# Kernel tuning notes

Hardware: AMD Instinct MI355X
Metric: run time of the kernel (lower is better)

The kernel has to match this reference:

```python
import jax, jax.numpy as jnp
import numpy as np


def setup_inputs() -> dict:
    key = jax.random.key(0)
    k1, k2 = jax.random.split(key)
    sites = jax.random.normal(k1, (4096, 128), dtype=jnp.float32)
    consensus = jax.random.normal(k2, (512, 128), dtype=jnp.float32)
    return {"sites": sites, "consensus": consensus}


def reference(sites, consensus):
    # Broadcast L1 distance: [N, 1, d] - [1, M, d] -> reduce |.| over d -> [N, M]
    dist = jnp.sum(jnp.abs(sites[:, None, :] - consensus[None, :, :]), axis=-1)
    # softmax over consensus axis of negated distances
    return jax.nn.softmax(-dist, axis=-1)
```

## Files before the change

kernel.cpp:

```cpp
#include <hip/hip_runtime.h>

#define N_SITES 4096
#define M_CONS  512
#define DIM     128
#define RPB     8
#define CH      16
#define NCH     8
#define QPC     4

__global__ __launch_bounds__(512, 1) void fused_kernel(const float* __restrict__ sites,
                                                       const float* __restrict__ cons,
                                                       float* __restrict__ out) {
    __shared__ __align__(16) float lds[16384];

    const int tid = threadIdx.x;
    const int bid = blockIdx.x;
    const int r0  = bid * RPB;

#pragma unroll
    for (int c = 0; c < 4; c++) {
        const int f = c * 512 + tid;
        const int r = f >> 2, q = f & 3;
        const float* gsrc = cons + (size_t)r * DIM + ((q ^ ((r >> 1) & 3)) << 2);
        __builtin_amdgcn_global_load_lds(
            (const __attribute__((address_space(1))) void*)gsrc,
            (__attribute__((address_space(3))) void*)&lds[f * 4], 16, 0, 0);
    }
    __syncthreads();

    float d[RPB];
#pragma unroll
    for (int i = 0; i < RPB; i++) d[i] = 0.f;

    const float* srow = sites + (size_t)r0 * DIM;

#pragma unroll
    for (int h = 0; h < NCH; h++) {
        float* cur = &lds[(h & 1) * 8192];
        float* nxt = &lds[((h + 1) & 1) * 8192];

        float cv[CH];
#pragma unroll
        for (int g = 0; g < QPC; g++) {
            float4 v = *(const float4*)&cur[tid * CH + ((g ^ ((tid >> 1) & 3)) << 2)];
            cv[4*g+0] = v.x; cv[4*g+1] = v.y; cv[4*g+2] = v.z; cv[4*g+3] = v.w;
        }

        if (h < NCH - 1) {
#pragma unroll
            for (int c = 0; c < 4; c++) {
                const int f = c * 512 + tid;
                const int r = f >> 2, q = f & 3;
                const float* gsrc = cons + (size_t)r * DIM + (h + 1) * CH
                                         + ((q ^ ((r >> 1) & 3)) << 2);
                __builtin_amdgcn_global_load_lds(
                    (const __attribute__((address_space(1))) void*)gsrc,
                    (__attribute__((address_space(3))) void*)&nxt[f * 4], 16, 0, 0);
            }
        }

#pragma unroll
        for (int rr = 0; rr < RPB; rr++) {
#pragma unroll
            for (int k = 0; k < CH; k++)
                d[rr] += fabsf(srow[rr * DIM + h * CH + k] - cv[k]);
        }

        __syncthreads();
    }

#pragma unroll
    for (int rr = 0; rr < RPB; rr++)
        lds[rr * 512 + tid] = d[rr];
    __syncthreads();

    const int wv = tid >> 6;
    const int ln = tid & 63;
    {
        const float* p = &lds[wv * 512 + ln * 8];
        float4 a = *(const float4*)(p);
        float4 b = *(const float4*)(p + 4);
        float m = fminf(fminf(fminf(a.x, a.y), fminf(a.z, a.w)),
                        fminf(fminf(b.x, b.y), fminf(b.z, b.w)));
#pragma unroll
        for (int off = 32; off > 0; off >>= 1) m = fminf(m, __shfl_xor(m, off));
        float s = ((__expf(m - a.x) + __expf(m - a.y)) + (__expf(m - a.z) + __expf(m - a.w)))
                + ((__expf(m - b.x) + __expf(m - b.y)) + (__expf(m - b.z) + __expf(m - b.w)));
#pragma unroll
        for (int off = 32; off > 0; off >>= 1) s += __shfl_xor(s, off);
        if (ln == 0) {
            lds[4096 + wv] = m;
            lds[4104 + wv] = 1.f / s;
        }
    }
    __syncthreads();

#pragma unroll
    for (int rr = 0; rr < RPB; rr++) {
        float mn  = lds[4096 + rr];
        float inv = lds[4104 + rr];
        out[(size_t)(r0 + rr) * M_CONS + tid] = __expf(mn - d[rr]) * inv;
    }
}

extern "C" void kernel_launch(void* const* d_in, const int* in_sizes, int n_in,
                              void* d_out, int out_size, void* d_ws, size_t ws_size,
                              hipStream_t stream) {
    const float* sites = (const float*)d_in[0];
    const float* cons  = (const float*)d_in[1];
    float* out = (float*)d_out;

    fused_kernel<<<N_SITES / RPB, 512, 0, stream>>>(sites, cons, out);
}
```

Before: 21.46 us.

## Make consensus staging wave-private and replace block barriers with waitcnt

Each wave now loads only the 64 consensus rows it consumes into its own LDS region, double-buffered with a prefetch distance of two chunks. The per-chunk __syncthreads is replaced by explicit vmcnt/lgkmcnt waits, so waves no longer synchronise with each other during the distance loop. This removes block-wide barrier stalls, at the cost of relying on hand-written waitcnt counts and on the compiler's ordering of the sites global loads.

Result: no change. 21.39 us (-0.3%).

```diff
diff --git a/kernel.cpp b/kernel.cpp
--- a/kernel.cpp
+++ b/kernel.cpp
@@ -6,7 +6,6 @@
 #define RPB     8
 #define CH      16
 #define NCH     8
-#define QPC     4
 
 __global__ __launch_bounds__(512, 1) void fused_kernel(const float* __restrict__ sites,
                                                        const float* __restrict__ cons,
@@ -16,47 +15,49 @@
     const int tid = threadIdx.x;
     const int bid = blockIdx.x;
     const int r0  = bid * RPB;
+    const int wv  = tid >> 6;
+    const int ln  = tid & 63;
 
+    float* wbase = &lds[wv * 2048];
+
+    auto issue = [&](int h, int b) {
+        float* dst = wbase + b * 1024;
 #pragma unroll
-    for (int c = 0; c < 4; c++) {
-        const int f = c * 512 + tid;
-        const int r = f >> 2, q = f & 3;
-        const float* gsrc = cons + (size_t)r * DIM + ((q ^ ((r >> 1) & 3)) << 2);
-        __builtin_amdgcn_global_load_lds(
-            (const __attribute__((address_space(1))) void*)gsrc,
-            (__attribute__((address_space(3))) void*)&lds[f * 4], 16, 0, 0);
-    }
-    __syncthreads();
+        for (int it = 0; it < 4; it++) {
+            const int f = it * 64 + ln;
+            const int c = f >> 2, q = f & 3;
+            const float* gsrc = cons + (size_t)(wv * 64 + c) * DIM + h * CH
+                                     + ((q ^ ((c >> 1) & 3)) << 2);
+            __builtin_amdgcn_global_load_lds(
+                (const __attribute__((address_space(1))) void*)gsrc,
+                (__attribute__((address_space(3))) void*)&dst[f * 4], 16, 0, 0);
+        }
+    };
+
+    issue(0, 0);
+    issue(1, 1);
 
     float d[RPB];
 #pragma unroll
     for (int i = 0; i < RPB; i++) d[i] = 0.f;
 
     const float* srow = sites + (size_t)r0 * DIM;
+    const int key = (ln >> 1) & 3;
 
 #pragma unroll
     for (int h = 0; h < NCH; h++) {
-        float* cur = &lds[(h & 1) * 8192];
-        float* nxt = &lds[((h + 1) & 1) * 8192];
+        if (h < NCH - 1) {
+            asm volatile("s_waitcnt vmcnt(4)" ::: "memory");
+        } else {
+            asm volatile("s_waitcnt vmcnt(0)" ::: "memory");
+        }
 
+        const float* B = wbase + (h & 1) * 1024;
         float cv[CH];
 #pragma unroll
-        for (int g = 0; g < QPC; g++) {
-            float4 v = *(const float4*)&cur[tid * CH + ((g ^ ((tid >> 1) & 3)) << 2)];
+        for (int g = 0; g < 4; g++) {
+            float4 v = *(const float4*)&B[ln * 16 + ((g ^ key) << 2)];
             cv[4*g+0] = v.x; cv[4*g+1] = v.y; cv[4*g+2] = v.z; cv[4*g+3] = v.w;
-        }
-
-        if (h < NCH - 1) {
-#pragma unroll
-            for (int c = 0; c < 4; c++) {
-                const int f = c * 512 + tid;
-                const int r = f >> 2, q = f & 3;
-                const float* gsrc = cons + (size_t)r * DIM + (h + 1) * CH
-                                         + ((q ^ ((r >> 1) & 3)) << 2);
-                __builtin_amdgcn_global_load_lds(
-                    (const __attribute__((address_space(1))) void*)gsrc,
-                    (__attribute__((address_space(3))) void*)&nxt[f * 4], 16, 0, 0);
-            }
         }
 
 #pragma unroll
@@ -66,16 +67,18 @@
                 d[rr] += fabsf(srow[rr * DIM + h * CH + k] - cv[k]);
         }
 
-        __syncthreads();
+        if (h < NCH - 2) {
+            asm volatile("s_waitcnt lgkmcnt(0)" ::: "memory");
+            issue(h + 2, h & 1);
+        }
     }
 
+    __syncthreads();
 #pragma unroll
     for (int rr = 0; rr < RPB; rr++)
         lds[rr * 512 + tid] = d[rr];
     __syncthreads();
 
-    const int wv = tid >> 6;
-    const int ln = tid & 63;
     {
         const float* p = &lds[wv * 512 + ln * 8];
         float4 a = *(const float4*)(p);
```
